# Performance work log

Measured on AMD Instinct MI355X. Metric: run time of the kernel, lower is better.

The kernel has to match this reference:

```python
import jax, jax.numpy as jnp
import numpy as np

N = 100000
IN_C, HID_C, OUT_C = 128, 128, 64
E = 1600000


def setup_inputs() -> dict:
    key = jax.random.key(0)
    ks = jax.random.split(key, 8)
    x = jax.random.normal(ks[0], (N, IN_C), dtype=jnp.float32)
    edge_index = jax.random.randint(ks[1], (2, E), 0, N, dtype=jnp.int64)
    def glorot(k, fan_in, fan_out):
        lim = np.sqrt(6.0 / (fan_in + fan_out)).astype(np.float32)
        return jax.random.uniform(k, (fan_in, fan_out), jnp.float32, -lim, lim)
    return {
        "x": x,
        "edge_index": edge_index,
        "W1l": glorot(ks[2], IN_C, HID_C),   # lin_l: aggregated neighbors
        "W1r": glorot(ks[3], IN_C, HID_C),   # lin_r: root/self
        "b1": jnp.zeros((HID_C,), jnp.float32),
        "W2l": glorot(ks[4], HID_C, OUT_C),
        "W2r": glorot(ks[5], HID_C, OUT_C),
        "b2": jnp.zeros((OUT_C,), jnp.float32),
    }


def _sage_conv(x, src, dst, Wl, Wr, b):
    # mean aggregation over incoming edges: gather source feats, segment-sum at dst
    msg_sum = jax.ops.segment_sum(x[src], dst, num_segments=N)          # [N, C_in]
    deg = jax.ops.segment_sum(jnp.ones((src.shape[0],), x.dtype), dst,
                              num_segments=N)                           # [N]
    mean = msg_sum / jnp.clip(deg, 1.0, None)[:, None]
    return mean @ Wl + x @ Wr + b


def reference(x, edge_index, W1l, W1r, b1, W2l, W2r, b2):
    src, dst = edge_index[0], edge_index[1]
    h = jax.nn.relu(_sage_conv(x, src, dst, W1l, W1r, b1))
    out = _sage_conv(h, src, dst, W2l, W2r, b2)
    return out
```

## Files before the change

kernel.cpp:

```cpp
#include <hip/hip_runtime.h>
#include <type_traits>


constexpr int K = 128;
constexpr int EB = 4096;

typedef __bf16 bf16x2 __attribute__((ext_vector_type(2)));
typedef __bf16 bf16x4 __attribute__((ext_vector_type(4)));
typedef __bf16 bf16x8 __attribute__((ext_vector_type(8)));
typedef float f32x4 __attribute__((ext_vector_type(4)));
typedef float f32x2 __attribute__((ext_vector_type(2)));


__device__ __forceinline__ unsigned char to_fp8(float v) {
#if __has_builtin(__builtin_amdgcn_cvt_pk_fp8_f32)
  int p = __builtin_amdgcn_cvt_pk_fp8_f32(v, v, 0, false);
  return (unsigned char)(p & 0xff);
#else
  unsigned u = __builtin_bit_cast(unsigned, v);
  unsigned s = (u >> 24) & 0x80u;
  float a = fabsf(v);
  if (a > 448.f) a = 448.f;
  unsigned bits;
  if (a < 0.015625f) {
    bits = (unsigned)(a * 512.f + 0.5f);
  } else {
    unsigned b = __builtin_bit_cast(unsigned, a);
    b += ((b >> 20) & 1) + 0x0007FFFF;
    unsigned e = (b >> 23) - 120;
    bits = (e << 3) | ((b >> 20) & 7);
    if (bits > 0x7E) bits = 0x7E;
  }
  return (unsigned char)(s | bits);
#endif
}

__device__ __forceinline__ f32x2 from_fp8x2(unsigned short u) {
#if __has_builtin(__builtin_amdgcn_cvt_pk_f32_fp8)
  return __builtin_amdgcn_cvt_pk_f32_fp8((int)u, false);
#else
  f32x2 r;
  unsigned b0 = u & 0xff, b1 = (u >> 8) & 0xff;
  unsigned e0 = (b0 >> 3) & 15, m0 = b0 & 7;
  unsigned e1 = (b1 >> 3) & 15, m1 = b1 & 7;
  float v0 = e0 ? __builtin_bit_cast(float, ((e0 + 120) << 23) | (m0 << 20))
              : (float)m0 * 0.001953125f;
  float v1 = e1 ? __builtin_bit_cast(float, ((e1 + 120) << 23) | (m1 << 20))
              : (float)m1 * 0.001953125f;
  r[0] = (b0 & 0x80) ? -v0 : v0;
  r[1] = (b1 & 0x80) ? -v1 : v1;
  return r;
#endif
}

__device__ __forceinline__ f32x2 fp8x2_lo(unsigned v) {
#if __has_builtin(__builtin_amdgcn_cvt_pk_f32_fp8)
  return __builtin_amdgcn_cvt_pk_f32_fp8((int)v, false);
#else
  return from_fp8x2((unsigned short)(v & 0xffffu));
#endif
}

__device__ __forceinline__ f32x2 fp8x2_hi(unsigned v) {
#if __has_builtin(__builtin_amdgcn_cvt_pk_f32_fp8)
  return __builtin_amdgcn_cvt_pk_f32_fp8((int)v, true);
#else
  return from_fp8x2((unsigned short)(v >> 16));
#endif
}


__global__ __launch_bounds__(256) void k_wprep_all(
    const float* __restrict__ W1l, const float* __restrict__ W1r,
    const float* __restrict__ W2l, const float* __restrict__ W2r,
    __bf16* __restrict__ B1l, __bf16* __restrict__ B1r,
    __bf16* __restrict__ B2l, __bf16* __restrict__ B2r) {
  int b = blockIdx.x;
  const float* W;
  __bf16* Bt;
  int idx;
  bool wide;
  if (b < 64) {
    W = W1l; Bt = B1l; idx = b * 256 + threadIdx.x; wide = true;
  } else if (b < 128) {
    W = W1r; Bt = B1r; idx = (b - 64) * 256 + threadIdx.x; wide = true;
  } else if (b < 160) {
    W = W2l; Bt = B2l; idx = (b - 128) * 256 + threadIdx.x; wide = false;
  } else {
    W = W2r; Bt = B2r; idx = (b - 160) * 256 + threadIdx.x; wide = false;
  }
  int k = wide ? (idx >> 7) : (idx >> 6);
  int c = wide ? (idx & 127) : (idx & 63);
  Bt[c * K + k] = (__bf16)W[idx];
}


__global__ __launch_bounds__(256) void k_bhist(const int* __restrict__ dst,
                                               int* __restrict__ blockHist,
                                               int* __restrict__ bucketTotal,
                                               int E, int n, int nB) {
  extern __shared__ int hist[];
  for (int i = threadIdx.x; i < nB; i += 256) hist[i] = 0;
  __syncthreads();
  int base = blockIdx.x * EB, end = min(base + EB, E);
  for (int e = base + threadIdx.x; e < end; e += 256) {
    int d = dst[e];
    if ((unsigned)d < (unsigned)n) atomicAdd(&hist[d >> 8], 1);
  }
  __syncthreads();
  for (int i = threadIdx.x; i < nB; i += 256) {
    int v = hist[i];
    blockHist[(long)blockIdx.x * nB + i] = v;
    if (v) atomicAdd(&bucketTotal[i], v);
  }
}

__global__ __launch_bounds__(512) void k_btop(const int* __restrict__ bucketTotal,
                                              int* __restrict__ bucketBase,
                                              int* __restrict__ bucketCursor, int nB) {
  __shared__ int sh[512];
  int t = threadIdx.x;
  int s = (t < nB) ? bucketTotal[t] : 0;
  sh[t] = s;
  __syncthreads();
  for (int off = 1; off < 512; off <<= 1) {
    int v = (t >= off) ? sh[t - off] : 0;
    __syncthreads();
    sh[t] += v;
    __syncthreads();
  }
  if (t < nB) {
    int base = sh[t] - s;
    bucketBase[t] = base;
    bucketCursor[t] = base;
    if (t == nB - 1) bucketBase[nB] = sh[t];
  }
}

__global__ __launch_bounds__(256) void k_bscatter(const int* __restrict__ src,
                                                  const int* __restrict__ dst,
                                                  const int* __restrict__ blockHist,
                                                  int* __restrict__ bucketCursor,
                                                  unsigned* __restrict__ recs,
                                                  int E, int n, int nB) {
  extern __shared__ int cur[];
  for (int i = threadIdx.x; i < nB; i += 256) {
    int c = blockHist[(long)blockIdx.x * nB + i];
    cur[i] = c ? atomicAdd(&bucketCursor[i], c) : 0;
  }
  __syncthreads();
  int base = blockIdx.x * EB, end = min(base + EB, E);
  for (int e = base + threadIdx.x; e < end; e += 256) {
    int d = dst[e];
    if ((unsigned)d < (unsigned)n) {
      int s = min(max(src[e], 0), n - 1);
      int pos = atomicAdd(&cur[d >> 8], 1);
      recs[pos] = ((unsigned)s << 8) | (unsigned)(d & 255);
    }
  }
}

__global__ __launch_bounds__(256) void k_bfill(const unsigned* __restrict__ recs,
                                               const int* __restrict__ bucketBase,
                                               int* __restrict__ rowptr,
                                               int* __restrict__ col, int n, int nB) {
  __shared__ int degl[256];
  __shared__ int incl[256];
  int b = blockIdx.x, t = threadIdx.x;
  int rbeg = bucketBase[b], rend = bucketBase[b + 1];
  degl[t] = 0;
  __syncthreads();
  for (int i = rbeg + t; i < rend; i += 256)
    atomicAdd(&degl[recs[i] & 255], 1);
  __syncthreads();
  incl[t] = degl[t];
  __syncthreads();
  for (int off = 1; off < 256; off <<= 1) {
    int v = (t >= off) ? incl[t - off] : 0;
    __syncthreads();
    incl[t] += v;
    __syncthreads();
  }
  int excl = incl[t] - degl[t];
  int node = b * 256 + t;
  if (node <= n) rowptr[node] = rbeg + excl;
  __syncthreads();
  degl[t] = rbeg + excl;
  __syncthreads();
  for (int i = rbeg + t; i < rend; i += 256) {
    unsigned r = recs[i];
    int pos = atomicAdd(&degl[r & 255], 1);
    col[pos] = (int)(r >> 8);
  }
}


template <int COLS, typename TIN>
__global__ __launch_bounds__(512, 4) void k_gemm_fused(const TIN* __restrict__ X,
                                                       const __bf16* __restrict__ Bta,
                                                       const __bf16* __restrict__ Btb,
                                                       unsigned char* __restrict__ outA,
                                                       __bf16* __restrict__ outB, int nrows) {
  constexpr int LD = 136;
  constexpr int NI = COLS / 64;
  __shared__ __bf16 As[64 * LD];

  int tid = threadIdx.x;
  long row0 = (long)blockIdx.x * 64;

  int w = tid >> 6, lane = tid & 63;
  int m = lane & 15, quad = lane >> 4;
  int panel = w >> 2;
  int wcol = (w & 3) * (16 * NI);
  const __bf16* Btg = panel ? Btb : Bta;

  bf16x8 bq[4][NI];
#pragma unroll
  for (int kc = 0; kc < 4; ++kc)
#pragma unroll
    for (int ni = 0; ni < NI; ++ni)
      bq[kc][ni] = *(const bf16x8*)(Btg + (long)(wcol + ni * 16 + m) * K + kc * 32 + quad * 8);

  if constexpr (std::is_same_v<TIN, float>) {
#pragma unroll
    for (int it = 0; it < 4; ++it) {
      int i = tid + it * 512;
      int r = i >> 5, c4 = (i & 31) << 2;
      long row = row0 + r;
      float4 v = make_float4(0.f, 0.f, 0.f, 0.f);
      if (row < nrows) v = *(const float4*)(X + row * K + c4);
      bf16x4 bb;
      bb[0] = (__bf16)v.x; bb[1] = (__bf16)v.y; bb[2] = (__bf16)v.z; bb[3] = (__bf16)v.w;
      *(bf16x4*)&As[r * LD + c4] = bb;
    }
  } else {
#pragma unroll
    for (int it = 0; it < 2; ++it) {
      int i = tid + it * 512;
      int r = i >> 4, c8 = (i & 15) << 3;
      long row = row0 + r;
      bf16x8 v = {};
      if (row < nrows) v = *(const bf16x8*)(X + row * K + c8);
      *(bf16x8*)&As[r * LD + c8] = v;
    }
  }

#pragma unroll
  for (int kc = 0; kc < 4; ++kc)
#pragma unroll
    for (int ni = 0; ni < NI; ++ni)
      asm volatile("" :: "v"(bq[kc][ni]));

  __syncthreads();

  f32x4 acc[4][NI];
#pragma unroll
  for (int mi = 0; mi < 4; ++mi)
#pragma unroll
    for (int ni = 0; ni < NI; ++ni) acc[mi][ni] = (f32x4){0.f, 0.f, 0.f, 0.f};

#pragma unroll
  for (int kc = 0; kc < 4; ++kc) {
    int ko = kc * 32 + quad * 8;
    bf16x8 af[4];
#pragma unroll
    for (int mi = 0; mi < 4; ++mi)
      af[mi] = *(const bf16x8*)&As[(mi * 16 + m) * LD + ko];
#pragma unroll
    for (int mi = 0; mi < 4; ++mi)
#pragma unroll
      for (int ni = 0; ni < NI; ++ni)
        acc[mi][ni] = __builtin_amdgcn_mfma_f32_16x16x32_bf16(af[mi], bq[kc][ni], acc[mi][ni], 0, 0, 0);
  }

#pragma unroll
  for (int mi = 0; mi < 4; ++mi) {
#pragma unroll
    for (int r = 0; r < 4; ++r) {
      long grow = row0 + mi * 16 + quad * 4 + r;
      if (grow < nrows) {
#pragma unroll
        for (int ni = 0; ni < NI; ++ni) {
          long idx = grow * COLS + wcol + ni * 16 + m;
          float v = acc[mi][ni][r];
          if (panel == 0) outA[idx] = to_fp8(v);
          else            outB[idx] = (__bf16)v;
        }
      }
    }
  }
}


template <bool RELU>
__global__ __launch_bounds__(256) void k_agg128(const unsigned char* __restrict__ Y,
                                                const __bf16* __restrict__ XR,
                                                const float* __restrict__ bias,
                                                const int* __restrict__ rowptr,
                                                const int* __restrict__ col,
                                                __bf16* __restrict__ out, int nnodes) {
  int wave = threadIdx.x >> 6, lane = threadIdx.x & 63;
  int quarter = lane >> 4, l = lane & 15;
  int sb = lane & 48;
  int n = blockIdx.x * 16 + wave * 4 + quarter;
  bool valid = n < nnodes;
  int beg = 0, end = 0;
  if (valid) {
    beg = rowptr[n];
    end = rowptr[n + 1];
  }
  int co = l * 8;
  const unsigned char* Yc = Y + co;

  f32x2 av0 = {0.f, 0.f}, av1 = {0.f, 0.f}, av2 = {0.f, 0.f}, av3 = {0.f, 0.f};

  for (int base = beg; base < end; base += 16) {
    int cnt = min(end - base, 16);
    int idx = (l < cnt) ? col[base + l] : 0;
    int j = 0;
    for (; j + 3 < cnt; j += 4) {
      long s0 = (unsigned)__shfl(idx, sb + j);
      long s1 = (unsigned)__shfl(idx, sb + j + 1);
      long s2 = (unsigned)__shfl(idx, sb + j + 2);
      long s3 = (unsigned)__shfl(idx, sb + j + 3);
      uint2 v0 = *(const uint2*)(Yc + s0 * 128);
      uint2 v1 = *(const uint2*)(Yc + s1 * 128);
      uint2 v2 = *(const uint2*)(Yc + s2 * 128);
      uint2 v3 = *(const uint2*)(Yc + s3 * 128);
      av0 += fp8x2_lo(v0.x); av1 += fp8x2_hi(v0.x);
      av2 += fp8x2_lo(v0.y); av3 += fp8x2_hi(v0.y);
      av0 += fp8x2_lo(v1.x); av1 += fp8x2_hi(v1.x);
      av2 += fp8x2_lo(v1.y); av3 += fp8x2_hi(v1.y);
      av0 += fp8x2_lo(v2.x); av1 += fp8x2_hi(v2.x);
      av2 += fp8x2_lo(v2.y); av3 += fp8x2_hi(v2.y);
      av0 += fp8x2_lo(v3.x); av1 += fp8x2_hi(v3.x);
      av2 += fp8x2_lo(v3.y); av3 += fp8x2_hi(v3.y);
    }
    for (; j < cnt; ++j) {
      long s = (unsigned)__shfl(idx, sb + j);
      uint2 v = *(const uint2*)(Yc + s * 128);
      av0 += fp8x2_lo(v.x); av1 += fp8x2_hi(v.x);
      av2 += fp8x2_lo(v.y); av3 += fp8x2_hi(v.y);
    }
  }

  if (valid) {
    float inv = 1.f / (float)max(end - beg, 1);
    bf16x8 xv = *(const bf16x8*)(XR + (long)n * 128 + co);
    f32x4 b0 = *(const f32x4*)(bias + co);
    f32x4 b1 = *(const f32x4*)(bias + co + 4);
    float r0 = av0[0] * inv + (float)xv[0] + b0[0];
    float r1 = av0[1] * inv + (float)xv[1] + b0[1];
    float r2 = av1[0] * inv + (float)xv[2] + b0[2];
    float r3 = av1[1] * inv + (float)xv[3] + b0[3];
    float r4 = av2[0] * inv + (float)xv[4] + b1[0];
    float r5 = av2[1] * inv + (float)xv[5] + b1[1];
    float r6 = av3[0] * inv + (float)xv[6] + b1[2];
    float r7 = av3[1] * inv + (float)xv[7] + b1[3];
    if (RELU) {
      r0 = fmaxf(r0, 0.f); r1 = fmaxf(r1, 0.f);
      r2 = fmaxf(r2, 0.f); r3 = fmaxf(r3, 0.f);
      r4 = fmaxf(r4, 0.f); r5 = fmaxf(r5, 0.f);
      r6 = fmaxf(r6, 0.f); r7 = fmaxf(r7, 0.f);
    }
    bf16x8 o;
    o[0] = (__bf16)r0; o[1] = (__bf16)r1; o[2] = (__bf16)r2; o[3] = (__bf16)r3;
    o[4] = (__bf16)r4; o[5] = (__bf16)r5; o[6] = (__bf16)r6; o[7] = (__bf16)r7;
    *(bf16x8*)(out + (long)n * 128 + co) = o;
  }
}

__global__ __launch_bounds__(256) void k_agg64(const unsigned char* __restrict__ Y,
                                               const __bf16* __restrict__ XR,
                                               const float* __restrict__ bias,
                                               const int* __restrict__ rowptr,
                                               const int* __restrict__ col,
                                               float* __restrict__ out, int nnodes) {
  int wave = threadIdx.x >> 6, lane = threadIdx.x & 63;
  int quarter = lane >> 4, l = lane & 15;
  int sb = lane & 48;
  int n = blockIdx.x * 16 + wave * 4 + quarter;
  bool valid = n < nnodes;
  int beg = 0, end = 0;
  if (valid) {
    beg = rowptr[n];
    end = rowptr[n + 1];
  }
  int co = l * 4;
  const unsigned char* Yc = Y + co;

  f32x2 av0 = {0.f, 0.f}, av1 = {0.f, 0.f};

  for (int base = beg; base < end; base += 16) {
    int cnt = min(end - base, 16);
    int idx = (l < cnt) ? col[base + l] : 0;
    int j = 0;
    for (; j + 3 < cnt; j += 4) {
      long s0 = (unsigned)__shfl(idx, sb + j);
      long s1 = (unsigned)__shfl(idx, sb + j + 1);
      long s2 = (unsigned)__shfl(idx, sb + j + 2);
      long s3 = (unsigned)__shfl(idx, sb + j + 3);
      unsigned v0 = *(const unsigned*)(Yc + s0 * 64);
      unsigned v1 = *(const unsigned*)(Yc + s1 * 64);
      unsigned v2 = *(const unsigned*)(Yc + s2 * 64);
      unsigned v3 = *(const unsigned*)(Yc + s3 * 64);
      av0 += fp8x2_lo(v0); av1 += fp8x2_hi(v0);
      av0 += fp8x2_lo(v1); av1 += fp8x2_hi(v1);
      av0 += fp8x2_lo(v2); av1 += fp8x2_hi(v2);
      av0 += fp8x2_lo(v3); av1 += fp8x2_hi(v3);
    }
    for (; j < cnt; ++j) {
      long s = (unsigned)__shfl(idx, sb + j);
      unsigned v = *(const unsigned*)(Yc + s * 64);
      av0 += fp8x2_lo(v); av1 += fp8x2_hi(v);
    }
  }

  if (valid) {
    float inv = 1.f / (float)max(end - beg, 1);
    bf16x4 xv = *(const bf16x4*)(XR + (long)n * 64 + co);
    f32x4 bv = *(const f32x4*)(bias + co);
    f32x4 r;
    r[0] = av0[0] * inv + (float)xv[0] + bv[0];
    r[1] = av0[1] * inv + (float)xv[1] + bv[1];
    r[2] = av1[0] * inv + (float)xv[2] + bv[2];
    r[3] = av1[1] * inv + (float)xv[3] + bv[3];
    *(f32x4*)(out + (long)n * 64 + co) = r;
  }
}


extern "C" void kernel_launch(void* const* d_in, const int* in_sizes, int n_in,
                              void* d_out, int out_size, void* d_ws, size_t ws_size,
                              hipStream_t stream) {
  const float* x   = (const float*)d_in[0];
  const int*   ei  = (const int*)d_in[1];
  const float* W1l = (const float*)d_in[2];
  const float* W1r = (const float*)d_in[3];
  const float* b1  = (const float*)d_in[4];
  const float* W2l = (const float*)d_in[5];
  const float* W2r = (const float*)d_in[6];
  const float* b2  = (const float*)d_in[7];
  float* out = (float*)d_out;

  int N = in_sizes[0] / K;
  int E = in_sizes[1] / 2;
  const int* src = ei;
  const int* dst = ei + E;

  int nB = (N + 255) >> 8;
  int nblk = (E + EB - 1) / EB;

  char* ws = (char*)d_ws;
  size_t off = 0;
  auto alloc = [&](size_t bytes) {
    void* p = ws + off;
    off = (off + bytes + 255) & ~(size_t)255;
    return p;
  };
  int*      rowptr       = (int*)alloc(((size_t)N + 2) * 4);
  int*      col          = (int*)alloc((size_t)E * 4);
  int*      blockHist    = (int*)alloc((size_t)nblk * nB * 4);
  int*      bucketTotal  = (int*)alloc(((size_t)nB) * 4);
  int*      bucketBase   = (int*)alloc(((size_t)nB + 1) * 4);
  int*      bucketCursor = (int*)alloc((size_t)nB * 4);
  unsigned* recs         = (unsigned*)alloc((size_t)E * 4);
  unsigned char* y1      = (unsigned char*)alloc((size_t)N * 128);
  __bf16*   xr           = (__bf16*)alloc((size_t)N * 128 * 2);
  __bf16*   h            = (__bf16*)alloc((size_t)N * 128 * 2);
  __bf16*   Bt1l         = (__bf16*)alloc((size_t)128 * K * 2);
  __bf16*   Bt1r         = (__bf16*)alloc((size_t)128 * K * 2);
  __bf16*   Bt2l         = (__bf16*)alloc((size_t)64 * K * 2);
  __bf16*   Bt2r         = (__bf16*)alloc((size_t)64 * K * 2);
  unsigned char* y2 = y1;
  __bf16*   hr = xr;

  k_wprep_all<<<192, 256, 0, stream>>>(W1l, W1r, W2l, W2r, Bt1l, Bt1r, Bt2l, Bt2r);

  hipMemsetAsync(bucketTotal, 0, (size_t)nB * 4, stream);
  k_bhist<<<nblk, 256, nB * 4, stream>>>(dst, blockHist, bucketTotal, E, N, nB);
  k_btop<<<1, 512, 0, stream>>>(bucketTotal, bucketBase, bucketCursor, nB);
  k_bscatter<<<nblk, 256, nB * 4, stream>>>(src, dst, blockHist, bucketCursor, recs, E, N, nB);
  k_bfill<<<nB, 256, 0, stream>>>(recs, bucketBase, rowptr, col, N, nB);

  int gx = (N + 63) / 64;
  k_gemm_fused<128, float><<<gx, 512, 0, stream>>>(x, Bt1l, Bt1r, y1, xr, N);
  k_agg128<true><<<(N + 15) / 16, 256, 0, stream>>>(y1, xr, b1, rowptr, col, h, N);

  k_gemm_fused<64, __bf16><<<gx, 512, 0, stream>>>(h, Bt2l, Bt2r, y2, hr, N);
  k_agg64<<<(N + 15) / 16, 256, 0, stream>>>(y2, hr, b2, rowptr, col, out, N);
}
```

Measured before the change: 266.0 us.

## Make GEMM kernels persistent with register prefetch and double-buffered LDS

Launches a capped grid of 512 blocks that loop over 64-row tiles, loading the weight fragments into registers once per block. The next tile's input is prefetched into registers while the current tile's MFMAs run, and LDS is double-buffered. This aims to cut per-block weight reloads and overlap global loads with compute, at the cost of fewer resident blocks per CU and higher register pressure.

```diff
diff --git a/kernel.cpp b/kernel.cpp
--- a/kernel.cpp
+++ b/kernel.cpp
@@ -200,14 +200,14 @@
                                                        const __bf16* __restrict__ Bta,
                                                        const __bf16* __restrict__ Btb,
                                                        unsigned char* __restrict__ outA,
-                                                       __bf16* __restrict__ outB, int nrows) {
+                                                       __bf16* __restrict__ outB,
+                                                       int nrows, int ntiles) {
   constexpr int LD = 136;
   constexpr int NI = COLS / 64;
-  __shared__ __bf16 As[64 * LD];
+  constexpr bool FP32IN = std::is_same_v<TIN, float>;
+  __shared__ __bf16 As[2][64 * LD];
 
   int tid = threadIdx.x;
-  long row0 = (long)blockIdx.x * 64;
-
   int w = tid >> 6, lane = tid & 63;
   int m = lane & 15, quad = lane >> 4;
   int panel = w >> 2;
@@ -221,29 +221,58 @@
     for (int ni = 0; ni < NI; ++ni)
       bq[kc][ni] = *(const bf16x8*)(Btg + (long)(wcol + ni * 16 + m) * K + kc * 32 + quad * 8);
 
-  if constexpr (std::is_same_v<TIN, float>) {
-#pragma unroll
-    for (int it = 0; it < 4; ++it) {
-      int i = tid + it * 512;
-      int r = i >> 5, c4 = (i & 31) << 2;
-      long row = row0 + r;
-      float4 v = make_float4(0.f, 0.f, 0.f, 0.f);
-      if (row < nrows) v = *(const float4*)(X + row * K + c4);
-      bf16x4 bb;
-      bb[0] = (__bf16)v.x; bb[1] = (__bf16)v.y; bb[2] = (__bf16)v.z; bb[3] = (__bf16)v.w;
-      *(bf16x4*)&As[r * LD + c4] = bb;
-    }
-  } else {
-#pragma unroll
-    for (int it = 0; it < 2; ++it) {
-      int i = tid + it * 512;
-      int r = i >> 4, c8 = (i & 15) << 3;
-      long row = row0 + r;
-      bf16x8 v = {};
-      if (row < nrows) v = *(const bf16x8*)(X + row * K + c8);
-      *(bf16x8*)&As[r * LD + c8] = v;
-    }
-  }
+  float4 ra[4];
+  bf16x8 rb[2];
+
+  auto load_tile = [&](int t) {
+    long row0 = (long)t * 64;
+    if constexpr (FP32IN) {
+#pragma unroll
+      for (int it = 0; it < 4; ++it) {
+        int i = tid + it * 512;
+        int r = i >> 5, c4 = (i & 31) << 2;
+        long row = row0 + r;
+        float4 v = make_float4(0.f, 0.f, 0.f, 0.f);
+        if (row < nrows) v = *(const float4*)(X + row * K + c4);
+        ra[it] = v;
+      }
+    } else {
+#pragma unroll
+      for (int it = 0; it < 2; ++it) {
+        int i = tid + it * 512;
+        int r = i >> 4, c8 = (i & 15) << 3;
+        long row = row0 + r;
+        bf16x8 v = {};
+        if (row < nrows) v = *(const bf16x8*)(X + row * K + c8);
+        rb[it] = v;
+      }
+    }
+  };
+
+  auto write_tile = [&](int buf) {
+    if constexpr (FP32IN) {
+#pragma unroll
+      for (int it = 0; it < 4; ++it) {
+        int i = tid + it * 512;
+        int r = i >> 5, c4 = (i & 31) << 2;
+        bf16x4 bb;
+        bb[0] = (__bf16)ra[it].x; bb[1] = (__bf16)ra[it].y;
+        bb[2] = (__bf16)ra[it].z; bb[3] = (__bf16)ra[it].w;
+        *(bf16x4*)&As[buf][r * LD + c4] = bb;
+      }
+    } else {
+#pragma unroll
+      for (int it = 0; it < 2; ++it) {
+        int i = tid + it * 512;
+        int r = i >> 4, c8 = (i & 15) << 3;
+        *(bf16x8*)&As[buf][r * LD + c8] = rb[it];
+      }
+    }
+  };
+
+  int t = (int)blockIdx.x;
+  int stride = (int)gridDim.x;
+  if (t < ntiles) load_tile(t);
 
 #pragma unroll
   for (int kc = 0; kc < 4; ++kc)
@@ -251,43 +280,54 @@
     for (int ni = 0; ni < NI; ++ni)
       asm volatile("" :: "v"(bq[kc][ni]));
 
-  __syncthreads();
-
-  f32x4 acc[4][NI];
-#pragma unroll
-  for (int mi = 0; mi < 4; ++mi)
-#pragma unroll
-    for (int ni = 0; ni < NI; ++ni) acc[mi][ni] = (f32x4){0.f, 0.f, 0.f, 0.f};
-
-#pragma unroll
-  for (int kc = 0; kc < 4; ++kc) {
-    int ko = kc * 32 + quad * 8;
-    bf16x8 af[4];
+  int buf = 0;
+  while (t < ntiles) {
+    write_tile(buf);
+    __syncthreads();
+
+    int tn = t + stride;
+    if (tn < ntiles) load_tile(tn);
+
+    f32x4 acc[4][NI];
 #pragma unroll
     for (int mi = 0; mi < 4; ++mi)
-      af[mi] = *(const bf16x8*)&As[(mi * 16 + m) * LD + ko];
-#pragma unroll
-    for (int mi = 0; mi < 4; ++mi)
-#pragma unroll
-      for (int ni = 0; ni < NI; ++ni)
-        acc[mi][ni] = __builtin_amdgcn_mfma_f32_16x16x32_bf16(af[mi], bq[kc][ni], acc[mi][ni], 0, 0, 0);
-  }
-
-#pragma unroll
-  for (int mi = 0; mi < 4; ++mi) {
-#pragma unroll
-    for (int r = 0; r < 4; ++r) {
-      long grow = row0 + mi * 16 + quad * 4 + r;
-      if (grow < nrows) {
-#pragma unroll
-        for (int ni = 0; ni < NI; ++ni) {
-          long idx = grow * COLS + wcol + ni * 16 + m;
-          float v = acc[mi][ni][r];
-          if (panel == 0) outA[idx] = to_fp8(v);
-          else            outB[idx] = (__bf16)v;
+#pragma unroll
+      for (int ni = 0; ni < NI; ++ni) acc[mi][ni] = (f32x4){0.f, 0.f, 0.f, 0.f};
+
+#pragma unroll
+    for (int kc = 0; kc < 4; ++kc) {
+      int ko = kc * 32 + quad * 8;
+      bf16x8 af[4];
+#pragma unroll
+      for (int mi = 0; mi < 4; ++mi)
+        af[mi] = *(const bf16x8*)&As[buf][(mi * 16 + m) * LD + ko];
+#pragma unroll
+      for (int mi = 0; mi < 4; ++mi)
+#pragma unroll
+        for (int ni = 0; ni < NI; ++ni)
+          acc[mi][ni] = __builtin_amdgcn_mfma_f32_16x16x32_bf16(af[mi], bq[kc][ni], acc[mi][ni], 0, 0, 0);
+    }
+
+    long row0 = (long)t * 64;
+#pragma unroll
+    for (int mi = 0; mi < 4; ++mi) {
+#pragma unroll
+      for (int r = 0; r < 4; ++r) {
+        long grow = row0 + mi * 16 + quad * 4 + r;
+        if (grow < nrows) {
+#pragma unroll
+          for (int ni = 0; ni < NI; ++ni) {
+            long idx = grow * COLS + wcol + ni * 16 + m;
+            float v = acc[mi][ni][r];
+            if (panel == 0) outA[idx] = to_fp8(v);
+            else            outB[idx] = (__bf16)v;
+          }
         }
       }
     }
+
+    t = tn;
+    buf ^= 1;
   }
 }
 
@@ -483,10 +523,11 @@
   k_bscatter<<<nblk, 256, nB * 4, stream>>>(src, dst, blockHist, bucketCursor, recs, E, N, nB);
   k_bfill<<<nB, 256, 0, stream>>>(recs, bucketBase, rowptr, col, N, nB);
 
-  int gx = (N + 63) / 64;
-  k_gemm_fused<128, float><<<gx, 512, 0, stream>>>(x, Bt1l, Bt1r, y1, xr, N);
+  int ntiles = (N + 63) / 64;
+  int gpers = ntiles < 512 ? ntiles : 512;
+  k_gemm_fused<128, float><<<gpers, 512, 0, stream>>>(x, Bt1l, Bt1r, y1, xr, N, ntiles);
   k_agg128<true><<<(N + 15) / 16, 256, 0, stream>>>(y1, xr, b1, rowptr, col, h, N);
 
-  k_gemm_fused<64, __bf16><<<gx, 512, 0, stream>>>(h, Bt2l, Bt2r, y2, hr, N);
+  k_gemm_fused<64, __bf16><<<gpers, 512, 0, stream>>>(h, Bt2l, Bt2r, y2, hr, N, ntiles);
   k_agg64<<<(N + 15) / 16, 256, 0, stream>>>(y2, hr, b2, rowptr, col, out, N);
 }
```

Result: no change. 267.0 us (+0.4%).
